# Kernel tuning notes

Measured on AMD Instinct MI355X. Metric: run time of the kernel, lower is better.

The kernel has to match this reference:

```python
import jax, jax.numpy as jnp
import numpy as np

B, T, E, H, V = 128, 400, 128, 128, 50000
H2, H4, H6 = 2 * H, 4 * H, 6 * H


def setup_inputs() -> dict:
    key = jax.random.key(0)
    ks = jax.random.split(key, 16)
    s = 0.05
    return dict(
        input_ids=jax.random.randint(ks[0], (B, 1), 0, V),
        pre_hidden=jax.random.normal(ks[1], (1, B, H2), jnp.float32),
        pre_cell=jax.random.normal(ks[2], (1, B, H2), jnp.float32),
        enc_outputs=jax.random.normal(ks[3], (B, T, H2), jnp.float32),
        source_input=jax.random.randint(ks[4], (B, T), 0, V),
        coverage=jax.random.uniform(ks[5], (B, 1, T), jnp.float32),
        emb_table=s * jax.random.normal(ks[6], (V, E), jnp.float32),
        w_ih=s * jax.random.normal(ks[7], (4 * H2, E), jnp.float32),
        w_hh=s * jax.random.normal(ks[8], (4 * H2, H2), jnp.float32),
        b_ih=jnp.zeros((4 * H2,), jnp.float32),
        b_hh=jnp.zeros((4 * H2,), jnp.float32),
        w_align=s * jax.random.normal(ks[9], (1, H6), jnp.float32),
        b_align=jnp.zeros((1,), jnp.float32),
        w_cov=s * jax.random.normal(ks[10], (H2, 1), jnp.float32),
        b_cov=jnp.zeros((H2,), jnp.float32),
        w_fc1=s * jax.random.normal(ks[11], (H4, H4), jnp.float32),
        b_fc1=jnp.zeros((H4,), jnp.float32),
        w_fc2=s * jax.random.normal(ks[12], (V, H4), jnp.float32),
        b_fc2=jnp.zeros((V,), jnp.float32),
        w_gen=s * jax.random.normal(ks[13], (1, H4 + E), jnp.float32),
        b_gen=jnp.zeros((1,), jnp.float32),
    )


def reference(input_ids, pre_hidden, pre_cell, enc_outputs, source_input, coverage,
              emb_table, w_ih, w_hh, b_ih, b_hh, w_align, b_align, w_cov, b_cov,
              w_fc1, b_fc1, w_fc2, b_fc2, w_gen, b_gen):
    # embedding lookup (flag=False path: no dropout)
    emb = emb_table[input_ids[:, 0]]                      # [B,E]
    # single-step LSTM (PyTorch gate order i,f,g,o; hidden size 2H)
    h0, c0 = pre_hidden[0], pre_cell[0]                   # [B,2H]
    gates = emb @ w_ih.T + b_ih + h0 @ w_hh.T + b_hh      # [B,8H]
    i, f, g, o = jnp.split(gates, 4, axis=-1)
    c = jax.nn.sigmoid(f) * c0 + jax.nn.sigmoid(i) * jnp.tanh(g)
    h = jax.nn.sigmoid(o) * jnp.tanh(c)                   # [B,2H]
    # coverage feature + attention over encoder steps
    cov_feat = coverage.transpose(0, 2, 1) @ w_cov.T + b_cov        # [B,T,2H]
    h_rep = jnp.broadcast_to(h[:, None, :], enc_outputs.shape)     # [B,T,2H]
    combine = jnp.concatenate([enc_outputs, h_rep, cov_feat], -1)  # [B,T,6H]
    scores = jnp.tanh(combine @ w_align.T + b_align)               # [B,T,1]
    attn = jax.nn.softmax(scores, axis=1)                          # [B,T,1]
    attn_bt = attn[:, :, 0]                                        # [B,T]
    cov_bt = coverage[:, 0, :]
    cov_loss = jnp.sum(jnp.minimum(attn_bt, cov_bt))
    new_cov = coverage + attn_bt[:, None, :]                       # [B,1,T]
    # context + vocab distribution
    context = jnp.einsum('bt,bte->be', attn_bt, enc_outputs)       # [B,2H]
    fc = jnp.tanh(jnp.concatenate([h, context], -1) @ w_fc1.T + b_fc1)
    pvocab = jax.nn.softmax(fc @ w_fc2.T + b_fc2, axis=1)          # [B,V]
    # copy distribution: fused batched scatter-add (replaces per-batch one-hot matmul loop)
    b_idx = jnp.arange(attn_bt.shape[0])[:, None]
    copy = jnp.zeros_like(pvocab).at[b_idx, source_input].add(attn_bt)
    # generation probability and mixture
    gen_in = jnp.concatenate([context, h, emb], -1)                # [B,4H+E]
    pgen = jax.nn.sigmoid(gen_in @ w_gen.T + b_gen)                # [B,1]
    out = pvocab * pgen + copy * (1.0 - pgen)
    return (out, h[None], c[None], attn_bt[:, None, :], copy, new_cov, cov_loss)
```

## Files before the change

### kernel.cpp

```cpp
#include <hip/hip_runtime.h>
#include <hip/hip_bf16.h>
#include <math.h>

#define B_  128
#define T_  400
#define E_  128
#define H2_ 256
#define H4_ 512
#define V_  50000
#define G4_ 1024
#define KACT 384

#define OFF_H       6400000
#define OFF_C       6432768
#define OFF_ATTN    6465536
#define OFF_COPY    6516736
#define OFF_NEWCOV 12916736
#define OFF_COVLOSS 12967936

#define WS_ACT   0
#define WS_GATES (WS_ACT + KACT*B_)
#define WS_HC    (WS_GATES + G4_*B_)
#define WS_FCB   (WS_HC + H4_*B_)
#define WS_SC    (WS_FCB + H4_*B_/2)
#define WS_ATTN  (WS_SC + B_*T_)
#define WS_CTXP  (WS_ATTN + B_*T_)
#define WS_SMP   (WS_CTXP + B_*8*H2_)
#define WS_HDOT  (WS_SMP + B_*8*2)
#define WS_COVP  (WS_HDOT + B_)
#define WS_PGEN  (WS_COVP + B_)
#define WS_MAX   (WS_PGEN + B_)
#define WS_INV   (WS_MAX + B_)
#define WS_AB    (WS_INV + B_)
#define WS_P0    (WS_AB + 16)
#define WS_P1    (WS_P0 + B_*V_)

typedef __attribute__((ext_vector_type(8))) short bf16x8;
typedef __attribute__((ext_vector_type(4))) float f32x4;
typedef __attribute__((ext_vector_type(16))) float f32x16;

__device__ inline float sigmoidf_(float x){ return 1.f/(1.f+__expf(-x)); }

__device__ inline short f2bf(float x){
  __hip_bfloat16 h = __float2bfloat16(x);
  return *reinterpret_cast<short*>(&h);
}

__device__ inline float blk_reduce_sum(float v, float* red){
  int t = threadIdx.x;
  red[t] = v; __syncthreads();
  for (int s = 128; s > 0; s >>= 1){ if (t < s) red[t] += red[t+s]; __syncthreads(); }
  float r = red[0]; __syncthreads(); return r;
}
__device__ inline float blk_reduce_max(float v, float* red){
  int t = threadIdx.x;
  red[t] = v; __syncthreads();
  for (int s = 128; s > 0; s >>= 1){ if (t < s) red[t] = fmaxf(red[t], red[t+s]); __syncthreads(); }
  float r = red[0]; __syncthreads(); return r;
}

__global__ __launch_bounds__(256) void k_zero(float* __restrict__ p){
  size_t i = ((size_t)blockIdx.x*256 + threadIdx.x)*4;
  if (i < (size_t)B_*V_)
    *(float4*)&p[i] = make_float4(0.f,0.f,0.f,0.f);
}

__global__ __launch_bounds__(256) void k_act(const int* __restrict__ ids,
    const float* __restrict__ pre_h, const float* __restrict__ emb_table,
    const float* __restrict__ w_align, const float* __restrict__ w_cov,
    const float* __restrict__ b_cov, float* __restrict__ act,
    float* __restrict__ ab){
  __shared__ float red[256];
  int t = threadIdx.x;
  int idx = blockIdx.x*256 + t;
  int k = idx >> 7, b = idx & 127;
  float v = (k < E_) ? emb_table[(size_t)ids[b]*E_ + k]
                     : pre_h[b*H2_ + (k - E_)];
  act[idx] = v;
  if (blockIdx.x == 0) {
    float wa = w_align[2*H2_ + t];
    float alpha = blk_reduce_sum(w_cov[t]*wa, red);
    float beta  = blk_reduce_sum(b_cov[t]*wa, red);
    if (t == 0) { ab[0] = alpha; ab[1] = beta; }
  }
}

__global__ __launch_bounds__(256) void k_gates(const float* __restrict__ act,
    const float* __restrict__ w_ih, const float* __restrict__ w_hh,
    const float* __restrict__ b_ih, const float* __restrict__ b_hh,
    float* __restrict__ gates){
  __shared__ float wt[8][KACT];
  int t = threadIdx.x; int j0 = blockIdx.x*8;
  for (int idx = t; idx < 8*KACT; idx += 256) {
    int r = idx / KACT, k = idx % KACT;
    int j = j0 + r;
    wt[r][k] = (k < E_) ? w_ih[j*E_ + k] : w_hh[j*H2_ + (k - E_)];
  }
  __syncthreads();
  int jq = t >> 7, b = t & 127;
  float acc[4] = {0.f,0.f,0.f,0.f};
  for (int k = 0; k < KACT; ++k) {
    float a = act[k*B_ + b];
    #pragma unroll
    for (int jj = 0; jj < 4; ++jj) acc[jj] += wt[jq*4+jj][k]*a;
  }
  #pragma unroll
  for (int jj = 0; jj < 4; ++jj) {
    int j = j0 + jq*4 + jj;
    gates[j*B_ + b] = acc[jj] + b_ih[j] + b_hh[j];
  }
}

__global__ __launch_bounds__(256) void k_lstm(const float* __restrict__ gates,
    const float* __restrict__ pre_c, const float* __restrict__ w_align,
    float* __restrict__ o_h, float* __restrict__ o_c,
    float* __restrict__ hc, float* __restrict__ hdot){
  __shared__ float red[256];
  int b = blockIdx.x, k = threadIdx.x;
  float i_ = gates[(0*H2_ + k)*B_ + b];
  float f_ = gates[(1*H2_ + k)*B_ + b];
  float g_ = gates[(2*H2_ + k)*B_ + b];
  float o_ = gates[(3*H2_ + k)*B_ + b];
  float c = sigmoidf_(f_)*pre_c[b*H2_ + k] + sigmoidf_(i_)*tanhf(g_);
  float h = sigmoidf_(o_)*tanhf(c);
  o_h[b*H2_ + k] = h;
  o_c[b*H2_ + k] = c;
  hc[k*B_ + b] = h;
  float s = blk_reduce_sum(h * w_align[H2_ + k], red);
  if (k == 0) hdot[b] = s;
}

__global__ __launch_bounds__(256) void k_scores(const float* __restrict__ enc,
    const float* __restrict__ cov, const float* __restrict__ w_align,
    const float* __restrict__ b_align, const float* __restrict__ hdot,
    const float* __restrict__ ab, float* __restrict__ sc){
  int b = blockIdx.y, c = blockIdx.x;
  int t = threadIdx.x, wave = t >> 6, lane = t & 63;
  float4 wa4 = *(const float4*)&w_align[lane*4];
  float hd = hdot[b], alpha = ab[0], beta = ab[1], ba = b_align[0];
  int t0 = c*50;
  for (int tt = t0 + wave; tt < t0 + 50; tt += 4) {
    const float4* ep = (const float4*)&enc[((size_t)b*T_ + tt)*H2_];
    float4 e4 = ep[lane];
    float d = e4.x*wa4.x + e4.y*wa4.y + e4.z*wa4.z + e4.w*wa4.w;
    #pragma unroll
    for (int m = 32; m >= 1; m >>= 1) d += __shfl_xor(d, m);
    if (lane == 0)
      sc[b*T_ + tt] = tanhf(d + hd + alpha*cov[b*T_ + tt] + beta + ba);
  }
}

__global__ __launch_bounds__(256) void k_soft(const float* __restrict__ sc_in,
    const float* __restrict__ cov, const int* __restrict__ src,
    float* __restrict__ o_attn, float* __restrict__ o_newcov,
    float* __restrict__ o_copy, float* __restrict__ covp,
    float* __restrict__ attn_ws){
  __shared__ float red[256];
  int b = blockIdx.x, t = threadIdx.x;
  float x1 = sc_in[b*T_ + t];
  float x2 = (t + 256 < T_) ? sc_in[b*T_ + t + 256] : -1e30f;
  float mx = blk_reduce_max(fmaxf(x1, x2), red);
  float e1 = __expf(x1 - mx);
  float e2 = (t + 256 < T_) ? __expf(x2 - mx) : 0.f;
  float sum = blk_reduce_sum(e1 + e2, red);
  float inv = 1.f/sum;
  float cl;
  {
    float a1 = e1*inv; float c1 = cov[b*T_ + t];
    attn_ws[b*T_ + t] = a1;
    o_attn[b*T_ + t] = a1;
    o_newcov[b*T_ + t] = c1 + a1;
    atomicAdd(&o_copy[(size_t)b*V_ + src[b*T_ + t]], a1);
    cl = fminf(a1, c1);
  }
  if (t + 256 < T_) {
    float a2 = e2*inv; float c2 = cov[b*T_ + t + 256];
    attn_ws[b*T_ + t + 256] = a2;
    o_attn[b*T_ + t + 256] = a2;
    o_newcov[b*T_ + t + 256] = c2 + a2;
    atomicAdd(&o_copy[(size_t)b*V_ + src[b*T_ + t + 256]], a2);
    cl += fminf(a2, c2);
  }
  float clsum = blk_reduce_sum(cl, red);
  if (t == 0) covp[b] = clsum;
}

__global__ __launch_bounds__(256) void k_ctx(const float* __restrict__ enc,
    const float* __restrict__ attn_ws, float* __restrict__ ctxp){
  __shared__ float a_s[50];
  int b = blockIdx.y, c = blockIdx.x, e = threadIdx.x;
  int t0 = c*50;
  if (e < 50) a_s[e] = attn_ws[b*T_ + t0 + e];
  __syncthreads();
  float acc = 0.f;
  #pragma unroll 5
  for (int i = 0; i < 50; ++i)
    acc += a_s[i] * enc[((size_t)b*T_ + t0 + i)*H2_ + e];
  ctxp[((size_t)b*8 + c)*H2_ + e] = acc;
}

__global__ __launch_bounds__(256) void k_ctxpgen(const float* __restrict__ ctxp,
    const int* __restrict__ ids, const float* __restrict__ emb_table,
    const float* __restrict__ w_gen, const float* __restrict__ b_gen,
    float* __restrict__ hc, float* __restrict__ pgen){
  __shared__ float red[256];
  int b = blockIdx.x, t = threadIdx.x;
  float ctx = 0.f;
  #pragma unroll
  for (int c = 0; c < 8; ++c) ctx += ctxp[((size_t)b*8 + c)*H2_ + t];
  hc[(H2_ + t)*B_ + b] = ctx;
  float p = ctx*w_gen[t] + hc[t*B_ + b]*w_gen[H2_ + t];
  if (t < E_) p += emb_table[(size_t)ids[b]*E_ + t]*w_gen[2*H2_ + t];
  float s = blk_reduce_sum(p, red);
  if (t == 0) pgen[b] = sigmoidf_(s + b_gen[0]);
}

__global__ __launch_bounds__(256) void k_fc1(const float* __restrict__ hc,
    const float* __restrict__ w_fc1, const float* __restrict__ b_fc1,
    short* __restrict__ fcb){
  __shared__ float wt[16][H4_];
  int t = threadIdx.x; int j0 = blockIdx.x*16;
  for (int idx = t; idx < 16*H4_; idx += 256) {
    int r = idx >> 9, k = idx & 511;
    wt[r][k] = w_fc1[(j0 + r)*H4_ + k];
  }
  __syncthreads();
  int jq = t >> 7, b = t & 127;
  float acc[8] = {};
  for (int k = 0; k < H4_; ++k) {
    float a = hc[k*B_ + b];
    #pragma unroll
    for (int jj = 0; jj < 8; ++jj) acc[jj] += wt[jq*8+jj][k]*a;
  }
  bf16x8 pack;
  #pragma unroll
  for (int jj = 0; jj < 8; ++jj) {
    int j = j0 + jq*8 + jj;
    pack[jj] = f2bf(tanhf(acc[jj] + b_fc1[j]));
  }
  *(bf16x8*)&fcb[(size_t)b*H4_ + j0 + jq*8] = pack;
}

#define KSH 256
__global__ __launch_bounds__(256, 2) void k_gemm2m(const short* __restrict__ fcb,
    const float* __restrict__ w_fc2, float* __restrict__ part){
  __shared__ short lds[B_*KSH];
  char* ldsb = (char*)lds;
  int t = threadIdx.x;
  int half = blockIdx.x & 1;
  int vt = blockIdx.x >> 1;
  int kb = half * KSH;
  int w = t >> 6, l = t & 63;
  int ln = l & 31, g2 = l >> 5;
  int v = vt*128 + w*32 + ln;
  int vc = v < V_ ? v : V_ - 1;

  #pragma unroll
  for (int r = 0; r < 16; ++r) {
    int lid = r*256 + t;
    int row = lid >> 5, cg = lid & 31;
    bf16x8 d = *(const bf16x8*)&fcb[row*H4_ + kb + cg*8];
    *(bf16x8*)(ldsb + row*512 + ((cg*16) ^ ((row & 31) << 4))) = d;
  }

  const float* wrow = w_fc2 + (size_t)vc*H4_ + kb + g2*8;
  f32x16 acc0 = {}, acc1 = {}, acc2 = {}, acc3 = {};

  #define LDQ(nm, s) float4 nm##a = *(const float4*)(wrow + (s)*16); \
                     float4 nm##b = *(const float4*)(wrow + (s)*16 + 4);
  #define STEPX(nm, s)                                                        \
  {                                                                           \
    bf16x8 bf;                                                                \
    bf[0]=f2bf(nm##a.x); bf[1]=f2bf(nm##a.y); bf[2]=f2bf(nm##a.z);            \
    bf[3]=f2bf(nm##a.w); bf[4]=f2bf(nm##b.x); bf[5]=f2bf(nm##b.y);            \
    bf[6]=f2bf(nm##b.z); bf[7]=f2bf(nm##b.w);                                 \
    int kbyte = (s)*32 + g2*16;                                               \
    { int row = ln;                                                           \
      bf16x8 af = *(const bf16x8*)(ldsb + row*512 + (kbyte ^ ((row&31)<<4))); \
      acc0 = __builtin_amdgcn_mfma_f32_32x32x16_bf16(af, bf, acc0, 0,0,0); }  \
    { int row = 32 + ln;                                                      \
      bf16x8 af = *(const bf16x8*)(ldsb + row*512 + (kbyte ^ ((row&31)<<4))); \
      acc1 = __builtin_amdgcn_mfma_f32_32x32x16_bf16(af, bf, acc1, 0,0,0); }  \
    { int row = 64 + ln;                                                      \
      bf16x8 af = *(const bf16x8*)(ldsb + row*512 + (kbyte ^ ((row&31)<<4))); \
      acc2 = __builtin_amdgcn_mfma_f32_32x32x16_bf16(af, bf, acc2, 0,0,0); }  \
    { int row = 96 + ln;                                                      \
      bf16x8 af = *(const bf16x8*)(ldsb + row*512 + (kbyte ^ ((row&31)<<4))); \
      acc3 = __builtin_amdgcn_mfma_f32_32x32x16_bf16(af, bf, acc3, 0,0,0); }  \
  }

  LDQ(q0,0) LDQ(q1,1) LDQ(q2,2) LDQ(q3,3)
  LDQ(q4,4) LDQ(q5,5) LDQ(q6,6) LDQ(q7,7)
  __syncthreads();
  LDQ(r0,8)   STEPX(q0,0)
  LDQ(r1,9)   STEPX(q1,1)
  LDQ(r2,10)  STEPX(q2,2)
  LDQ(r3,11)  STEPX(q3,3)
  LDQ(r4,12)  STEPX(q4,4)
  LDQ(r5,13)  STEPX(q5,5)
  LDQ(r6,14)  STEPX(q6,6)
  LDQ(r7,15)  STEPX(q7,7)
  STEPX(r0,8)
  STEPX(r1,9)
  STEPX(r2,10)
  STEPX(r3,11)
  STEPX(r4,12)
  STEPX(r5,13)
  STEPX(r6,14)
  STEPX(r7,15)
  #undef LDQ
  #undef STEPX

  if (v < V_) {
    float* pp = part + (size_t)half*B_*V_;
    #pragma unroll
    for (int r = 0; r < 16; ++r) {
      int brow = (r & 3) + 8*(r >> 2) + 4*g2;
      pp[(size_t)(brow)*V_ + v]      = acc0[r];
      pp[(size_t)(32 + brow)*V_ + v] = acc1[r];
      pp[(size_t)(64 + brow)*V_ + v] = acc2[r];
      pp[(size_t)(96 + brow)*V_ + v] = acc3[r];
    }
  }
}

__global__ __launch_bounds__(256) void k_smp(const float* __restrict__ p0,
    const float* __restrict__ p1, const float* __restrict__ b_fc2,
    float* __restrict__ logits, float* __restrict__ smp){
  __shared__ float rm[256], rs[256];
  int b = blockIdx.y, c = blockIdx.x, t = threadIdx.x;
  int v0 = c*6250, v1 = v0 + 6250;
  size_t base = (size_t)b*V_;
  float m = -1e30f, s = 0.f;
  for (int v = v0 + t*2; v < v1; v += 512) {
    float2 a0 = *(const float2*)&p0[base + v];
    float2 a1 = *(const float2*)&p1[base + v];
    float2 bb = *(const float2*)&b_fc2[v];
    float2 x;
    x.x = a0.x + a1.x + bb.x;
    x.y = a0.y + a1.y + bb.y;
    *(float2*)&logits[base + v] = x;
    float nm = fmaxf(m, fmaxf(x.x, x.y));
    s = s*__expf(m - nm) + __expf(x.x - nm) + __expf(x.y - nm);
    m = nm;
  }
  rm[t] = m; rs[t] = s; __syncthreads();
  for (int k = 128; k > 0; k >>= 1) {
    if (t < k) {
      float m1 = rm[t], s1 = rs[t], m2 = rm[t+k], s2 = rs[t+k];
      float nm = fmaxf(m1, m2);
      rm[t] = nm; rs[t] = s1*__expf(m1-nm) + s2*__expf(m2-nm);
    }
    __syncthreads();
  }
  if (t == 0) { smp[(b*8+c)*2] = rm[0]; smp[(b*8+c)*2+1] = rs[0]; }
}

__global__ __launch_bounds__(128) void k_smred_cl(const float* __restrict__ smp,
    const float* __restrict__ covp, float* __restrict__ mx,
    float* __restrict__ inv, float* __restrict__ o_cl){
  __shared__ float red[128];
  int t = threadIdx.x;
  float m = -1e30f, s = 0.f;
  #pragma unroll
  for (int c = 0; c < 8; ++c) {
    float m2 = smp[(t*8+c)*2], s2 = smp[(t*8+c)*2+1];
    float nm = fmaxf(m, m2);
    s = s*__expf(m - nm) + s2*__expf(m2 - nm);
    m = nm;
  }
  mx[t] = m; inv[t] = 1.f/s;
  red[t] = covp[t]; __syncthreads();
  for (int k = 64; k > 0; k >>= 1){ if (t < k) red[t] += red[t+k]; __syncthreads(); }
  if (t == 0) o_cl[0] = red[0];
}

__global__ __launch_bounds__(256) void k_final(const float* __restrict__ copy,
    const float* __restrict__ mx, const float* __restrict__ inv_s,
    const float* __restrict__ pgen, float* __restrict__ out){
  size_t gid = (size_t)blockIdx.x*256 + threadIdx.x;
  int b = (int)(gid / (V_/4));
  int v = (int)(gid % (V_/4))*4;
  size_t idx = (size_t)b*V_ + v;
  float m = mx[b], is = inv_s[b], pg = pgen[b];
  float4 lg = *(const float4*)&out[idx];
  float4 cp = *(const float4*)&copy[idx];
  float4 o;
  o.x = __expf(lg.x - m)*is*pg + cp.x*(1.f - pg);
  o.y = __expf(lg.y - m)*is*pg + cp.y*(1.f - pg);
  o.z = __expf(lg.z - m)*is*pg + cp.z*(1.f - pg);
  o.w = __expf(lg.w - m)*is*pg + cp.w*(1.f - pg);
  *(float4*)&out[idx] = o;
}

extern "C" void kernel_launch(void* const* d_in, const int* in_sizes, int n_in,
                              void* d_out, int out_size, void* d_ws, size_t ws_size,
                              hipStream_t stream) {
  const int*   ids       = (const int*)  d_in[0];
  const float* pre_h     = (const float*)d_in[1];
  const float* pre_c     = (const float*)d_in[2];
  const float* enc       = (const float*)d_in[3];
  const int*   src       = (const int*)  d_in[4];
  const float* cov       = (const float*)d_in[5];
  const float* emb_table = (const float*)d_in[6];
  const float* w_ih      = (const float*)d_in[7];
  const float* w_hh      = (const float*)d_in[8];
  const float* b_ih      = (const float*)d_in[9];
  const float* b_hh      = (const float*)d_in[10];
  const float* w_align   = (const float*)d_in[11];
  const float* b_align   = (const float*)d_in[12];
  const float* w_cov     = (const float*)d_in[13];
  const float* b_cov     = (const float*)d_in[14];
  const float* w_fc1     = (const float*)d_in[15];
  const float* b_fc1     = (const float*)d_in[16];
  const float* w_fc2     = (const float*)d_in[17];
  const float* b_fc2     = (const float*)d_in[18];
  const float* w_gen     = (const float*)d_in[19];
  const float* b_gen     = (const float*)d_in[20];

  float* out = (float*)d_out;
  float* ws  = (float*)d_ws;

  float* o_out    = out;
  float* o_h      = out + OFF_H;
  float* o_c      = out + OFF_C;
  float* o_attn   = out + OFF_ATTN;
  float* o_copy   = out + OFF_COPY;
  float* o_newcov = out + OFF_NEWCOV;
  float* o_cl     = out + OFF_COVLOSS;

  k_zero <<<(B_*V_/4 + 255)/256, 256, 0, stream>>>(o_copy);
  k_act  <<<192, 256, 0, stream>>>(ids, pre_h, emb_table, w_align, w_cov, b_cov,
                                   ws + WS_ACT, ws + WS_AB);
  k_gates<<<128, 256, 0, stream>>>(ws + WS_ACT, w_ih, w_hh, b_ih, b_hh, ws + WS_GATES);
  k_lstm <<<128, 256, 0, stream>>>(ws + WS_GATES, pre_c, w_align, o_h, o_c,
                                   ws + WS_HC, ws + WS_HDOT);
  k_scores<<<dim3(8,128), 256, 0, stream>>>(enc, cov, w_align, b_align,
                                   ws + WS_HDOT, ws + WS_AB, ws + WS_SC);
  k_soft <<<128, 256, 0, stream>>>(ws + WS_SC, cov, src, o_attn, o_newcov, o_copy,
                                   ws + WS_COVP, ws + WS_ATTN);
  k_ctx  <<<dim3(8,128), 256, 0, stream>>>(enc, ws + WS_ATTN, ws + WS_CTXP);
  k_ctxpgen<<<128, 256, 0, stream>>>(ws + WS_CTXP, ids, emb_table, w_gen, b_gen,
                                   ws + WS_HC, ws + WS_PGEN);
  k_fc1  <<<32, 256, 0, stream>>>(ws + WS_HC, w_fc1, b_fc1, (short*)(ws + WS_FCB));
  k_gemm2m<<<2*((V_ + 127)/128), 256, 0, stream>>>((const short*)(ws + WS_FCB),
                                   w_fc2, ws + WS_P0);
  k_smp  <<<dim3(8,128), 256, 0, stream>>>(ws + WS_P0, ws + WS_P1, b_fc2,
                                   o_out, ws + WS_SMP);
  k_smred_cl<<<1, 128, 0, stream>>>(ws + WS_SMP, ws + WS_COVP,
                                   ws + WS_MAX, ws + WS_INV, o_cl);
  k_final<<<(int)(((size_t)B_*V_/4)/256), 256, 0, stream>>>(
      o_copy, ws + WS_MAX, ws + WS_INV, ws + WS_PGEN, o_out);
}
```

Measured before the change: 165.0 us.

## Drop split-K partials in vocab GEMM, write biased logits directly

The vocab projection GEMM no longer splits K across two blocks writing separate partial buffers. Each block now loops over both K halves, restaging the activations in LDS between them, and writes logits with the bias added straight into the output. The softmax-stats kernel then reads a single logits array instead of two partials plus bias, removing a full B×V write and read of intermediate data. The trade-off is half as many GEMM blocks (about 391), each with a longer serial K loop and an extra barrier and LDS restage, which lowers parallelism.

```diff
diff --git a/kernel.cpp b/kernel.cpp
--- a/kernel.cpp
+++ b/kernel.cpp
@@ -32,8 +32,6 @@
 #define WS_MAX   (WS_PGEN + B_)
 #define WS_INV   (WS_MAX + B_)
 #define WS_AB    (WS_INV + B_)
-#define WS_P0    (WS_AB + 16)
-#define WS_P1    (WS_P0 + B_*V_)
 
 typedef __attribute__((ext_vector_type(8))) short bf16x8;
 typedef __attribute__((ext_vector_type(4))) float f32x4;
@@ -241,33 +239,37 @@
   *(bf16x8*)&fcb[(size_t)b*H4_ + j0 + jq*8] = pack;
 }
 
-#define KSH 256
+#define KH 256
 __global__ __launch_bounds__(256, 2) void k_gemm2m(const short* __restrict__ fcb,
-    const float* __restrict__ w_fc2, float* __restrict__ part){
-  __shared__ short lds[B_*KSH];
+    const float* __restrict__ w_fc2, const float* __restrict__ b_fc2,
+    float* __restrict__ logits){
+  __shared__ short lds[B_*KH];
   char* ldsb = (char*)lds;
   int t = threadIdx.x;
-  int half = blockIdx.x & 1;
-  int vt = blockIdx.x >> 1;
-  int kb = half * KSH;
   int w = t >> 6, l = t & 63;
   int ln = l & 31, g2 = l >> 5;
-  int v = vt*128 + w*32 + ln;
+  int v = blockIdx.x*128 + w*32 + ln;
   int vc = v < V_ ? v : V_ - 1;
-
-  #pragma unroll
-  for (int r = 0; r < 16; ++r) {
-    int lid = r*256 + t;
-    int row = lid >> 5, cg = lid & 31;
-    bf16x8 d = *(const bf16x8*)&fcb[row*H4_ + kb + cg*8];
-    *(bf16x8*)(ldsb + row*512 + ((cg*16) ^ ((row & 31) << 4))) = d;
-  }
-
-  const float* wrow = w_fc2 + (size_t)vc*H4_ + kb + g2*8;
+  const float* wrow0 = w_fc2 + (size_t)vc*H4_ + g2*8;
+  const float* wrow1 = wrow0 + KH;
   f32x16 acc0 = {}, acc1 = {}, acc2 = {}, acc3 = {};
 
-  #define LDQ(nm, s) float4 nm##a = *(const float4*)(wrow + (s)*16); \
-                     float4 nm##b = *(const float4*)(wrow + (s)*16 + 4);
+  float4 q0a,q0b,q1a,q1b,q2a,q2b,q3a,q3b,q4a,q4b,q5a,q5b,q6a,q6b,q7a,q7b;
+  float4 r0a,r0b,r1a,r1b,r2a,r2b,r3a,r3b,r4a,r4b,r5a,r5b,r6a,r6b,r7a,r7b;
+
+  #define SB __builtin_amdgcn_sched_barrier(0);
+  #define LDQ(nm, base, s) { nm##a = *(const float4*)((base) + (s)*16); \
+                             nm##b = *(const float4*)((base) + (s)*16 + 4); }
+  #define STAGE(h)                                                            \
+  {                                                                           \
+    _Pragma("unroll")                                                         \
+    for (int r = 0; r < 16; ++r) {                                            \
+      int lid = r*256 + t;                                                    \
+      int row = lid >> 5, cg = lid & 31;                                      \
+      bf16x8 d = *(const bf16x8*)&fcb[row*H4_ + (h)*KH + cg*8];               \
+      *(bf16x8*)(ldsb + row*512 + ((cg*16) ^ ((row & 31) << 4))) = d;         \
+    }                                                                         \
+  }
   #define STEPX(nm, s)                                                        \
   {                                                                           \
     bf16x8 bf;                                                                \
@@ -289,17 +291,39 @@
       acc3 = __builtin_amdgcn_mfma_f32_32x32x16_bf16(af, bf, acc3, 0,0,0); }  \
   }
 
-  LDQ(q0,0) LDQ(q1,1) LDQ(q2,2) LDQ(q3,3)
-  LDQ(q4,4) LDQ(q5,5) LDQ(q6,6) LDQ(q7,7)
-  __syncthreads();
-  LDQ(r0,8)   STEPX(q0,0)
-  LDQ(r1,9)   STEPX(q1,1)
-  LDQ(r2,10)  STEPX(q2,2)
-  LDQ(r3,11)  STEPX(q3,3)
-  LDQ(r4,12)  STEPX(q4,4)
-  LDQ(r5,13)  STEPX(q5,5)
-  LDQ(r6,14)  STEPX(q6,6)
-  LDQ(r7,15)  STEPX(q7,7)
+  STAGE(0)
+  LDQ(q0,wrow0,0) LDQ(q1,wrow0,1) LDQ(q2,wrow0,2) LDQ(q3,wrow0,3)
+  LDQ(q4,wrow0,4) LDQ(q5,wrow0,5) LDQ(q6,wrow0,6) LDQ(q7,wrow0,7)
+  SB
+  __syncthreads();
+  LDQ(r0,wrow0,8)  SB STEPX(q0,0)
+  LDQ(r1,wrow0,9)  SB STEPX(q1,1)
+  LDQ(r2,wrow0,10) SB STEPX(q2,2)
+  LDQ(r3,wrow0,11) SB STEPX(q3,3)
+  LDQ(r4,wrow0,12) SB STEPX(q4,4)
+  LDQ(r5,wrow0,13) SB STEPX(q5,5)
+  LDQ(r6,wrow0,14) SB STEPX(q6,6)
+  LDQ(r7,wrow0,15) SB STEPX(q7,7)
+  LDQ(q0,wrow1,0)  SB STEPX(r0,8)
+  LDQ(q1,wrow1,1)  SB STEPX(r1,9)
+  LDQ(q2,wrow1,2)  SB STEPX(r2,10)
+  LDQ(q3,wrow1,3)  SB STEPX(r3,11)
+  LDQ(q4,wrow1,4)  SB STEPX(r4,12)
+  LDQ(q5,wrow1,5)  SB STEPX(r5,13)
+  LDQ(q6,wrow1,6)  SB STEPX(r6,14)
+  LDQ(q7,wrow1,7)  SB STEPX(r7,15)
+  __syncthreads();
+  STAGE(1)
+  SB
+  __syncthreads();
+  LDQ(r0,wrow1,8)  SB STEPX(q0,0)
+  LDQ(r1,wrow1,9)  SB STEPX(q1,1)
+  LDQ(r2,wrow1,10) SB STEPX(q2,2)
+  LDQ(r3,wrow1,11) SB STEPX(q3,3)
+  LDQ(r4,wrow1,12) SB STEPX(q4,4)
+  LDQ(r5,wrow1,13) SB STEPX(q5,5)
+  LDQ(r6,wrow1,14) SB STEPX(q6,6)
+  LDQ(r7,wrow1,15) SB STEPX(q7,7)
   STEPX(r0,8)
   STEPX(r1,9)
   STEPX(r2,10)
@@ -308,40 +332,34 @@
   STEPX(r5,13)
   STEPX(r6,14)
   STEPX(r7,15)
+  #undef SB
   #undef LDQ
+  #undef STAGE
   #undef STEPX
 
   if (v < V_) {
-    float* pp = part + (size_t)half*B_*V_;
+    float bias = b_fc2[v];
     #pragma unroll
     for (int r = 0; r < 16; ++r) {
       int brow = (r & 3) + 8*(r >> 2) + 4*g2;
-      pp[(size_t)(brow)*V_ + v]      = acc0[r];
-      pp[(size_t)(32 + brow)*V_ + v] = acc1[r];
-      pp[(size_t)(64 + brow)*V_ + v] = acc2[r];
-      pp[(size_t)(96 + brow)*V_ + v] = acc3[r];
+      logits[(size_t)(brow)*V_ + v]      = acc0[r] + bias;
+      logits[(size_t)(32 + brow)*V_ + v] = acc1[r] + bias;
+      logits[(size_t)(64 + brow)*V_ + v] = acc2[r] + bias;
+      logits[(size_t)(96 + brow)*V_ + v] = acc3[r] + bias;
     }
   }
 }
 
-__global__ __launch_bounds__(256) void k_smp(const float* __restrict__ p0,
-    const float* __restrict__ p1, const float* __restrict__ b_fc2,
-    float* __restrict__ logits, float* __restrict__ smp){
+__global__ __launch_bounds__(256) void k_smp(const float* __restrict__ logits,
+    float* __restrict__ smp){
   __shared__ float rm[256], rs[256];
   int b = blockIdx.y, c = blockIdx.x, t = threadIdx.x;
   int v0 = c*6250, v1 = v0 + 6250;
-  size_t base = (size_t)b*V_;
   float m = -1e30f, s = 0.f;
-  for (int v = v0 + t*2; v < v1; v += 512) {
-    float2 a0 = *(const float2*)&p0[base + v];
-    float2 a1 = *(const float2*)&p1[base + v];
-    float2 bb = *(const float2*)&b_fc2[v];
-    float2 x;
-    x.x = a0.x + a1.x + bb.x;
-    x.y = a0.y + a1.y + bb.y;
-    *(float2*)&logits[base + v] = x;
-    float nm = fmaxf(m, fmaxf(x.x, x.y));
-    s = s*__expf(m - nm) + __expf(x.x - nm) + __expf(x.y - nm);
+  for (int v = v0 + t; v < v1; v += 256) {
+    float x = logits[(size_t)b*V_ + v];
+    float nm = fmaxf(m, x);
+    s = s*__expf(m - nm) + __expf(x - nm);
     m = nm;
   }
   rm[t] = m; rs[t] = s; __syncthreads();
@@ -443,10 +461,9 @@
   k_ctxpgen<<<128, 256, 0, stream>>>(ws + WS_CTXP, ids, emb_table, w_gen, b_gen,
                                    ws + WS_HC, ws + WS_PGEN);
   k_fc1  <<<32, 256, 0, stream>>>(ws + WS_HC, w_fc1, b_fc1, (short*)(ws + WS_FCB));
-  k_gemm2m<<<2*((V_ + 127)/128), 256, 0, stream>>>((const short*)(ws + WS_FCB),
-                                   w_fc2, ws + WS_P0);
-  k_smp  <<<dim3(8,128), 256, 0, stream>>>(ws + WS_P0, ws + WS_P1, b_fc2,
-                                   o_out, ws + WS_SMP);
+  k_gemm2m<<<(V_ + 127)/128, 256, 0, stream>>>((const short*)(ws + WS_FCB),
+                                   w_fc2, b_fc2, o_out);
+  k_smp  <<<dim3(8,128), 256, 0, stream>>>(o_out, ws + WS_SMP);
   k_smred_cl<<<1, 128, 0, stream>>>(ws + WS_SMP, ws + WS_COVP,
                                    ws + WS_MAX, ws + WS_INV, o_cl);
   k_final<<<(int)(((size_t)B_*V_/4)/256), 256, 0, stream>>>(
```

After: 159.9 us. 3.1% less time.
